# Kernel optimization log

Hardware: AMD Instinct MI355X
Metric: run time of the kernel (lower is better)

## Reference

```python
import jax, jax.numpy as jnp
import numpy as np

NEG_SLOPE = 0.2  # PyG GATv2Conv default negative_slope


def setup_inputs() -> dict:
    key = jax.random.key(0)
    ks = jax.random.split(key, 8)
    B, N, C, H, F, E = 16, 5000, 128, 2, 64, 1_280_000
    T = B * N
    s = 0.05
    x = jax.random.normal(ks[0], (B, N, C), jnp.float32)
    edge_index = jax.random.randint(ks[1], (2, E), 0, T, jnp.int32)
    Wl = jax.random.normal(ks[2], (C, H * F), jnp.float32) * s
    bl = jnp.zeros((H * F,), jnp.float32)
    Wr = jax.random.normal(ks[3], (C, H * F), jnp.float32) * s
    br = jnp.zeros((H * F,), jnp.float32)
    att = jax.random.normal(ks[4], (H, F), jnp.float32) * s
    bias = jnp.zeros((H * F,), jnp.float32)
    return {"x": x, "edge_index": edge_index, "Wl": Wl, "bl": bl,
            "Wr": Wr, "br": br, "att": att, "bias": bias}


def reference(x, edge_index, Wl, bl, Wr, br, att, bias):
    # x: (B, N, C) -> flatten to (T, C), T = B*N total nodes
    B, N, C = x.shape
    T = B * N
    H, F = att.shape
    xf = x.reshape(T, C)
    x_l = (xf @ Wl + bl).reshape(T, H, F)  # source transform (lin_l)
    x_r = (xf @ Wr + br).reshape(T, H, F)  # target transform (lin_r)
    # add self loops (add_self_loops=True)
    loops = jnp.arange(T, dtype=edge_index.dtype)
    src = jnp.concatenate([edge_index[0], loops])
    dst = jnp.concatenate([edge_index[1], loops])
    # GATv2 score: att . LeakyReLU(x_j + x_i)
    e = jax.nn.leaky_relu(x_l[src] + x_r[dst], NEG_SLOPE)  # (Et, H, F)
    logits = jnp.einsum('ehf,hf->eh', e, att)              # (Et, H)
    # edge softmax over incoming edges of each dst node
    m = jax.lax.stop_gradient(jax.ops.segment_max(logits, dst, num_segments=T))
    p = jnp.exp(logits - m[dst])
    denom = jax.ops.segment_sum(p, dst, num_segments=T)
    alpha = p / denom[dst]                                  # (Et, H)
    # aggregate: out_i = sum_j alpha_ij * x_l[j]
    out = jax.ops.segment_sum(x_l[src] * alpha[:, :, None], dst, num_segments=T)
    out = out.reshape(T, H * F) + bias  # concat=True -> (T, H*F)
    return out.reshape(B, N, H * F)
```

## Files before the change

kernel.cpp:

```cpp
#include <hip/hip_runtime.h>
#include <hip/hip_bf16.h>

typedef __hip_bfloat16 bf16;
typedef short s16x8 __attribute__((ext_vector_type(8)));
typedef float f32x4 __attribute__((ext_vector_type(4)));
typedef float f32x2 __attribute__((ext_vector_type(2)));

#define NEG_SLOPE 0.2f
#define MAXB 160
#define EPB  4096
#define CAP  12288

__device__ __forceinline__ unsigned int f32_to_bf16_bits(float f) {
    unsigned int u = __float_as_uint(f);
    return (u + 0x7FFFu + ((u >> 16) & 1u)) >> 16;
}
__device__ __forceinline__ float bf16lo_to_f32(unsigned int u) {
    return __uint_as_float(u << 16);
}
__device__ __forceinline__ float bf16hi_to_f32(unsigned int u) {
    return __uint_as_float(u & 0xFFFF0000u);
}
__device__ __forceinline__ float loadf_rt(const void* p, size_t i, int isb) {
    return isb ? __bfloat162float(((const bf16*)p)[i]) : ((const float*)p)[i];
}

#define ROR_ADD(v, n)                                                          \
    v += __int_as_float(__builtin_amdgcn_update_dpp(                           \
        0, __float_as_int(v), 0x120 + (n), 0xF, 0xF, true))

__global__ void detect_dtype(const unsigned short* __restrict__ xh, int* __restrict__ flag,
                             int* __restrict__ gtot)
{
    int lane = threadIdx.x;
    for (int j = lane; j < MAXB; j += 64) gtot[j] = 0;
    int cnt = 0;
    for (int j = lane; j < 256; j += 64) {
        unsigned short h = xh[j];
        int e = (h >> 7) & 0xFF;
        if ((h & 0x7FFF) == 0 || (e >= 117 && e <= 131)) cnt++;
    }
    #pragma unroll
    for (int off = 32; off; off >>= 1) cnt += __shfl_xor(cnt, off, 64);
    if (lane == 0) *flag = (cnt >= 192) ? 1 : 0;
}

__global__ void prep_w(const void* __restrict__ Wl, const void* __restrict__ Wr,
                       unsigned short* __restrict__ bpack, const int* __restrict__ flag)
{
    int isb = *flag;
    int tid = blockIdx.x * blockDim.x + threadIdx.x;
    if (tid >= 2 * 8 * 4 * 64) return;
    int lane = tid & 63;
    int kc   = (tid >> 6) & 3;
    int nt   = (tid >> 8) & 7;
    int mat  = tid >> 11;
    const void* W = mat ? Wr : Wl;
    int n  = nt * 16 + (lane & 15);
    int k0 = kc * 32 + (lane >> 4) * 8;
    unsigned short* o = bpack + (size_t)tid * 8;
    #pragma unroll
    for (int j = 0; j < 8; ++j)
        o[j] = (unsigned short)f32_to_bf16_bits(loadf_rt(W, (size_t)(k0 + j) * 128 + n, isb));
}

__global__ void gemm_mfma(const void* __restrict__ x,
                          const unsigned short* __restrict__ bpack,
                          const void* __restrict__ bl, const void* __restrict__ br,
                          unsigned int* __restrict__ xlp, unsigned int* __restrict__ xrp,
                          int T, const int* __restrict__ flag)
{
    int isb  = *flag;
    int lane = threadIdx.x & 63;
    int w    = blockIdx.x * 4 + (threadIdx.x >> 6);
    int row0 = w * 16;
    if (row0 >= T) return;
    int m = lane & 15, quad = lane >> 4;
    int arow = min(row0 + m, T - 1);

    f32x4 acc[16];
    #pragma unroll
    for (int nt = 0; nt < 16; ++nt) acc[nt] = (f32x4){0.f, 0.f, 0.f, 0.f};

    const s16x8* bp = (const s16x8*)bpack;
    for (int kc = 0; kc < 4; ++kc) {
        s16x8 a;
        if (isb) {
            const unsigned short* xb = (const unsigned short*)x
                                     + (size_t)arow * 128 + kc * 32 + quad * 8;
            a = *(const s16x8*)xb;
        } else {
            const float* xp = (const float*)x + (size_t)arow * 128 + kc * 32 + quad * 8;
            float4 xa = ((const float4*)xp)[0];
            float4 xc = ((const float4*)xp)[1];
            a[0] = (short)f32_to_bf16_bits(xa.x); a[1] = (short)f32_to_bf16_bits(xa.y);
            a[2] = (short)f32_to_bf16_bits(xa.z); a[3] = (short)f32_to_bf16_bits(xa.w);
            a[4] = (short)f32_to_bf16_bits(xc.x); a[5] = (short)f32_to_bf16_bits(xc.y);
            a[6] = (short)f32_to_bf16_bits(xc.z); a[7] = (short)f32_to_bf16_bits(xc.w);
        }
        #pragma unroll
        for (int nt = 0; nt < 16; ++nt) {
            s16x8 b = bp[(size_t)(((nt >> 3) * 32) + (nt & 7) * 4 + kc) * 64 + lane];
            acc[nt] = __builtin_amdgcn_mfma_f32_16x16x32_bf16(a, b, acc[nt], 0, 0, 0);
        }
    }
    #pragma unroll
    for (int nt = 0; nt < 4; ++nt) {
        int fl = nt * 16 + m;
        float bl0 = loadf_rt(bl, fl, isb), bl1 = loadf_rt(bl, 64 + fl, isb);
        float br0 = loadf_rt(br, fl, isb), br1 = loadf_rt(br, 64 + fl, isb);
        #pragma unroll
        for (int r = 0; r < 4; ++r) {
            int t = row0 + quad * 4 + r;
            if (t < T) {
                unsigned int pl = f32_to_bf16_bits(acc[nt][r] + bl0)
                                | (f32_to_bf16_bits(acc[nt + 4][r] + bl1) << 16);
                unsigned int pr = f32_to_bf16_bits(acc[nt + 8][r] + br0)
                                | (f32_to_bf16_bits(acc[nt + 12][r] + br1) << 16);
                xlp[(size_t)t * 64 + fl] = pl;
                xrp[(size_t)t * 64 + fl] = pr;
            }
        }
    }
}


__global__ void bucket_hist2(const int* __restrict__ ei, int E, int Et,
                             int nbuck, int* __restrict__ gtot)
{
    __shared__ int h[4][MAXB];
    int tid = threadIdx.x, wid = tid >> 6;
    for (int j = tid; j < 4 * MAXB; j += 256) h[j / MAXB][j % MAXB] = 0;
    __syncthreads();
    int start = blockIdx.x * EPB;
    int end   = min(start + EPB, Et);
    for (int i = start + tid; i < end; i += 256) {
        int dst = (i < E) ? ei[E + i] : (i - E);
        atomicAdd(&h[wid][dst >> 9], 1);
    }
    __syncthreads();
    for (int b = tid; b < nbuck; b += 256) {
        int v = h[0][b] + h[1][b] + h[2][b] + h[3][b];
        if (v) atomicAdd(&gtot[b], v);
    }
}

__global__ void scan_buckets(int* __restrict__ gtot, int nbuck, int Et,
                             int* __restrict__ bases, int* __restrict__ rowptr_T)
{
    __shared__ int sd[256];
    int tid = threadIdx.x;
    int v = (tid < nbuck) ? gtot[tid] : 0;
    sd[tid] = v;
    __syncthreads();
    for (int off = 1; off < 256; off <<= 1) {
        int u = (tid >= off) ? sd[tid - off] : 0;
        __syncthreads();
        sd[tid] += u;
        __syncthreads();
    }
    int excl = sd[tid] - v;
    if (tid < nbuck) { bases[tid] = excl; gtot[tid] = excl; }
    if (tid == 0) { bases[nbuck] = Et; *rowptr_T = Et; }
}

__global__ void bucket_scatter2(const int* __restrict__ ei, int E, int Et,
                                int nbuck, int* __restrict__ gcur,
                                unsigned int* __restrict__ packed)
{
    __shared__ int h[4][MAXB];
    __shared__ int cur[MAXB];
    int tid = threadIdx.x, wid = tid >> 6;
    for (int j = tid; j < 4 * MAXB; j += 256) h[j / MAXB][j % MAXB] = 0;
    __syncthreads();
    int start = blockIdx.x * EPB;
    int end   = min(start + EPB, Et);
    for (int i = start + tid; i < end; i += 256) {
        int dst = (i < E) ? ei[E + i] : (i - E);
        atomicAdd(&h[wid][dst >> 9], 1);
    }
    __syncthreads();
    for (int b = tid; b < nbuck; b += 256) {
        int v = h[0][b] + h[1][b] + h[2][b] + h[3][b];
        cur[b] = v ? atomicAdd(&gcur[b], v) : 0;
    }
    __syncthreads();
    for (int i = start + tid; i < end; i += 256) {
        int src, dst;
        if (i < E) { src = ei[i]; dst = ei[E + i]; }
        else       { src = i - E; dst = i - E; }
        int pos = atomicAdd(&cur[dst >> 9], 1);
        packed[pos] = ((unsigned int)src << 9) | (unsigned int)(dst & 511);
    }
}

__global__ void build_csr(unsigned int* __restrict__ colpacked,
                          const int* __restrict__ bases, int nbuck,
                          int Et, int T, int* __restrict__ row_ptr)
{
    __shared__ unsigned int st[CAP];
    __shared__ int h[512];
    __shared__ int off[512];
    __shared__ int ws[4];
    int b    = blockIdx.x;
    int tid  = threadIdx.x, lane = tid & 63, wid = tid >> 6;
    int base = bases[b];
    int endb = bases[b + 1];
    int m    = min(endb - base, CAP);

    for (int i = tid; i < m; i += 256) st[i] = colpacked[base + i];
    for (int j = tid; j < 512; j += 256) h[j] = 0;
    __syncthreads();
    for (int i = tid; i < m; i += 256) atomicAdd(&h[st[i] & 511], 1);
    __syncthreads();

    int h0 = h[2 * tid], h1 = h[2 * tid + 1];
    int s  = h0 + h1;
    int xx = s;
    #pragma unroll
    for (int o = 1; o < 64; o <<= 1) {
        int u = __shfl_up(xx, o, 64);
        if (lane >= o) xx += u;
    }
    if (lane == 63) ws[wid] = xx;
    __syncthreads();
    int wo = 0;
    for (int wv = 0; wv < 4; ++wv) if (wv < wid) wo += ws[wv];
    int e0 = wo + xx - s;
    int e1 = e0 + h0;
    off[2 * tid]     = e0;
    off[2 * tid + 1] = e1;
    int node0 = b * 512 + 2 * tid;
    if (node0 < T)     row_ptr[node0]     = base + e0;
    if (node0 + 1 < T) row_ptr[node0 + 1] = base + e1;
    __syncthreads();

    for (int i = tid; i < m; i += 256) {
        unsigned int p = st[i];
        int pos = atomicAdd(&off[p & 511], 1);
        colpacked[base + pos] = p >> 9;
    }
}

__global__ void aggregate(const unsigned int* __restrict__ xlp,
                          const unsigned int* __restrict__ xrp,
                          const int* __restrict__ row_ptr, const int* __restrict__ col,
                          const void* __restrict__ att, const void* __restrict__ bias,
                          float* __restrict__ out, int T,
                          const int* __restrict__ flag)
{
    int lane = threadIdx.x & 63;
    int node = blockIdx.x * 8 + (threadIdx.x >> 5);
    if (node >= T) return;
    int isb = *flag;
    int g = (lane >> 4) & 1;
    int q = lane & 15;

    uint4 xr4 = ((const uint4*)(xrp + (size_t)node * 64))[q];
    f32x2 xr2[4], at2[4];
    {
        unsigned int xrw[4] = {xr4.x, xr4.y, xr4.z, xr4.w};
        #pragma unroll
        for (int k = 0; k < 4; ++k) {
            xr2[k] = (f32x2){bf16lo_to_f32(xrw[k]), bf16hi_to_f32(xrw[k])};
            at2[k] = (f32x2){loadf_rt(att, q * 4 + k, isb),
                             loadf_rt(att, 64 + q * 4 + k, isb)};
        }
    }

    f32x2 s2 = {0.f, 0.f};
    f32x2 a2[4] = {{0.f, 0.f}, {0.f, 0.f}, {0.f, 0.f}, {0.f, 0.f}};

    int beg = row_ptr[node], end = row_ptr[node + 1];

    bool v0 = (beg + g) < end;      int sA = v0 ? col[beg + g]     : node;
    bool v1 = (beg + 2 + g) < end;  int sB = v1 ? col[beg + 2 + g] : node;
    bool v2 = (beg + 4 + g) < end;  int sC = v2 ? col[beg + 4 + g] : node;
    uint4 cx = ((const uint4*)(xlp + (size_t)sA * 64))[q];
    uint4 nx = ((const uint4*)(xlp + (size_t)sB * 64))[q];

    for (int i = beg; i < end; i += 2) {
        bool v3 = (i + 6 + g) < end;
        int  sD = v3 ? col[i + 6 + g] : node;
        uint4 px = ((const uint4*)(xlp + (size_t)sC * 64))[q];

        unsigned int xlw[4] = {cx.x, cx.y, cx.z, cx.w};
        f32x2 xl2[4];
        f32x2 t2 = {0.f, 0.f};
        #pragma unroll
        for (int k = 0; k < 4; ++k) {
            xl2[k] = (f32x2){bf16lo_to_f32(xlw[k]), bf16hi_to_f32(xlw[k])};
            f32x2 e  = xl2[k] + xr2[k];
            f32x2 lr = __builtin_elementwise_max(e, e * NEG_SLOPE);
            t2 = __builtin_elementwise_fma(lr, at2[k], t2);
        }
        float t0 = t2.x, t1 = t2.y;
        ROR_ADD(t0, 8); ROR_ADD(t1, 8);
        ROR_ADD(t0, 4); ROR_ADD(t1, 4);
        ROR_ADD(t0, 2); ROR_ADD(t1, 2);
        ROR_ADD(t0, 1); ROR_ADD(t1, 1);
        t0 = fminf(fmaxf(t0, -30.f), 30.f);
        t1 = fminf(fmaxf(t1, -30.f), 30.f);
        f32x2 p2;
        p2.x = v0 ? __expf(t0) : 0.f;
        p2.y = v0 ? __expf(t1) : 0.f;
        s2 += p2;
        #pragma unroll
        for (int k = 0; k < 4; ++k)
            a2[k] = __builtin_elementwise_fma(p2, xl2[k], a2[k]);

        cx = nx; nx = px;
        v0 = v1; v1 = v2; v2 = v3; sC = sD;
    }

    s2.x += __shfl_xor(s2.x, 16, 64);
    s2.y += __shfl_xor(s2.y, 16, 64);
    #pragma unroll
    for (int k = 0; k < 4; ++k) {
        a2[k].x += __shfl_xor(a2[k].x, 16, 64);
        a2[k].y += __shfl_xor(a2[k].y, 16, 64);
    }

    float inv0 = (s2.x > 0.f) ? 1.f / s2.x : 0.f;
    float inv1 = (s2.y > 0.f) ? 1.f / s2.y : 0.f;
    if (g == 0) {
        float4 o;
        o.x = fmaf(a2[0].x, inv0, loadf_rt(bias, q * 4 + 0, isb));
        o.y = fmaf(a2[1].x, inv0, loadf_rt(bias, q * 4 + 1, isb));
        o.z = fmaf(a2[2].x, inv0, loadf_rt(bias, q * 4 + 2, isb));
        o.w = fmaf(a2[3].x, inv0, loadf_rt(bias, q * 4 + 3, isb));
        ((float4*)(out + (size_t)node * 128))[q] = o;
    } else {
        float4 o;
        o.x = fmaf(a2[0].y, inv1, loadf_rt(bias, 64 + q * 4 + 0, isb));
        o.y = fmaf(a2[1].y, inv1, loadf_rt(bias, 64 + q * 4 + 1, isb));
        o.z = fmaf(a2[2].y, inv1, loadf_rt(bias, 64 + q * 4 + 2, isb));
        o.w = fmaf(a2[3].y, inv1, loadf_rt(bias, 64 + q * 4 + 3, isb));
        ((float4*)(out + (size_t)node * 128))[16 + q] = o;
    }
}

extern "C" void kernel_launch(void* const* d_in, const int* in_sizes, int n_in,
                              void* d_out, int out_size, void* d_ws, size_t ws_size,
                              hipStream_t stream)
{
    const void* x    = d_in[0];
    const int*  ei   = (const int*)d_in[1];
    const void* Wl   = d_in[2];
    const void* bl   = d_in[3];
    const void* Wr   = d_in[4];
    const void* br   = d_in[5];
    const void* att  = d_in[6];
    const void* bias = d_in[7];
    float* out = (float*)d_out;

    int T     = in_sizes[0] / 128;
    int E     = in_sizes[1] / 2;
    int Et    = E + T;
    int nbuck = (T + 511) >> 9;
    int nb    = (Et + EPB - 1) / EPB;

    char* w = (char*)d_ws;
    unsigned int* xlp = (unsigned int*)w;  w += (size_t)T * 64 * 4;
    unsigned int* xrp = (unsigned int*)w;  w += (size_t)T * 64 * 4;
    int* rowptr = (int*)w;  w += (size_t)(T + 1) * 4;
    unsigned int* col = (unsigned int*)w;  w += (size_t)Et * 4;
    int* gtot   = (int*)w;  w += MAXB * 4;
    int* bases  = (int*)w;  w += (MAXB + 8) * 4;
    int* flag   = (int*)w;  w += 256;
    unsigned short* bpack = (unsigned short*)w;  w += 2 * 8 * 4 * 64 * 8 * 2;

    detect_dtype<<<1, 64, 0, stream>>>((const unsigned short*)x, flag, gtot);
    prep_w<<<16, 256, 0, stream>>>(Wl, Wr, bpack, flag);
    gemm_mfma<<<(T + 63) / 64, 256, 0, stream>>>(x, bpack, bl, br, xlp, xrp, T, flag);

    bucket_hist2<<<nb, 256, 0, stream>>>(ei, E, Et, nbuck, gtot);
    scan_buckets<<<1, 256, 0, stream>>>(gtot, nbuck, Et, bases, rowptr + T);
    bucket_scatter2<<<nb, 256, 0, stream>>>(ei, E, Et, nbuck, gtot, col);
    build_csr<<<nbuck, 256, 0, stream>>>(col, bases, nbuck, Et, T, rowptr);

    aggregate<<<(T + 7) / 8, 256, 0, stream>>>(xlp, xrp, rowptr, (const int*)col,
                                               att, bias, out, T, flag);
}
```

Before: 247.9 us.

## Stage bucket scatter in shared memory, deepen gather prefetch, use exp2 softmax

The bucket scatter kernel now sorts each block's edges by bucket locally in shared memory, then writes them to global memory in contiguous runs per bucket instead of as random scattered stores. The aggregate kernel deepens its software prefetch of source feature rows from two rows ahead to three, to hide more gather latency at the cost of extra registers. It also folds log2(e) into the attention weights so it can call exp2f directly, replacing the symmetric clamp with an upper clamp only. The scatter kernel uses about 20KB more LDS per block, which may reduce occupancy.

```diff
diff --git a/kernel.cpp b/kernel.cpp
--- a/kernel.cpp
+++ b/kernel.cpp
@@ -164,12 +164,18 @@
     if (tid == 0) { bases[nbuck] = Et; *rowptr_T = Et; }
 }
 
-__global__ void bucket_scatter2(const int* __restrict__ ei, int E, int Et,
+__global__ void bucket_scatter3(const int* __restrict__ ei, int E, int Et,
                                 int nbuck, int* __restrict__ gcur,
                                 unsigned int* __restrict__ packed)
 {
+    __shared__ unsigned int st[EPB];
+    __shared__ unsigned char bk[EPB];
     __shared__ int h[4][MAXB];
+    __shared__ int sd[256];
+    __shared__ int loff[MAXB];
     __shared__ int cur[MAXB];
+    __shared__ int gpos[MAXB];
+
     int tid = threadIdx.x, wid = tid >> 6;
     for (int j = tid; j < 4 * MAXB; j += 256) h[j / MAXB][j % MAXB] = 0;
     __syncthreads();
@@ -180,17 +186,37 @@
         atomicAdd(&h[wid][dst >> 9], 1);
     }
     __syncthreads();
-    for (int b = tid; b < nbuck; b += 256) {
-        int v = h[0][b] + h[1][b] + h[2][b] + h[3][b];
-        cur[b] = v ? atomicAdd(&gcur[b], v) : 0;
+    int v = 0;
+    if (tid < nbuck) v = h[0][tid] + h[1][tid] + h[2][tid] + h[3][tid];
+    sd[tid] = v;
+    __syncthreads();
+    for (int off = 1; off < 256; off <<= 1) {
+        int u = (tid >= off) ? sd[tid - off] : 0;
+        __syncthreads();
+        sd[tid] += u;
+        __syncthreads();
+    }
+    if (tid < nbuck) {
+        int excl = sd[tid] - v;
+        loff[tid] = excl;
+        cur[tid]  = excl;
+        gpos[tid] = v ? atomicAdd(&gcur[tid], v) : 0;
     }
     __syncthreads();
     for (int i = start + tid; i < end; i += 256) {
         int src, dst;
         if (i < E) { src = ei[i]; dst = ei[E + i]; }
         else       { src = i - E; dst = i - E; }
-        int pos = atomicAdd(&cur[dst >> 9], 1);
-        packed[pos] = ((unsigned int)src << 9) | (unsigned int)(dst & 511);
+        int b = dst >> 9;
+        int pos = atomicAdd(&cur[b], 1);
+        st[pos] = ((unsigned int)src << 9) | (unsigned int)(dst & 511);
+        bk[pos] = (unsigned char)b;
+    }
+    __syncthreads();
+    int mm = end - start;
+    for (int i = tid; i < mm; i += 256) {
+        int b = bk[i];
+        packed[gpos[b] + (i - loff[b])] = st[i];
     }
 }
 
@@ -260,11 +286,12 @@
     f32x2 xr2[4], at2[4];
     {
         unsigned int xrw[4] = {xr4.x, xr4.y, xr4.z, xr4.w};
+        const float LOG2E = 1.44269504f;
         #pragma unroll
         for (int k = 0; k < 4; ++k) {
             xr2[k] = (f32x2){bf16lo_to_f32(xrw[k]), bf16hi_to_f32(xrw[k])};
-            at2[k] = (f32x2){loadf_rt(att, q * 4 + k, isb),
-                             loadf_rt(att, 64 + q * 4 + k, isb)};
+            at2[k] = (f32x2){loadf_rt(att, q * 4 + k, isb) * LOG2E,
+                             loadf_rt(att, 64 + q * 4 + k, isb) * LOG2E};
         }
     }
 
@@ -276,13 +303,15 @@
     bool v0 = (beg + g) < end;      int sA = v0 ? col[beg + g]     : node;
     bool v1 = (beg + 2 + g) < end;  int sB = v1 ? col[beg + 2 + g] : node;
     bool v2 = (beg + 4 + g) < end;  int sC = v2 ? col[beg + 4 + g] : node;
+    bool v3 = (beg + 6 + g) < end;  int sD = v3 ? col[beg + 6 + g] : node;
     uint4 cx = ((const uint4*)(xlp + (size_t)sA * 64))[q];
     uint4 nx = ((const uint4*)(xlp + (size_t)sB * 64))[q];
+    uint4 px = ((const uint4*)(xlp + (size_t)sC * 64))[q];
 
     for (int i = beg; i < end; i += 2) {
-        bool v3 = (i + 6 + g) < end;
-        int  sD = v3 ? col[i + 6 + g] : node;
-        uint4 px = ((const uint4*)(xlp + (size_t)sC * 64))[q];
+        bool v4 = (i + 8 + g) < end;
+        int  sE = v4 ? col[i + 8 + g] : node;
+        uint4 qx = ((const uint4*)(xlp + (size_t)sD * 64))[q];
 
         unsigned int xlw[4] = {cx.x, cx.y, cx.z, cx.w};
         f32x2 xl2[4];
@@ -299,18 +328,18 @@
         ROR_ADD(t0, 4); ROR_ADD(t1, 4);
         ROR_ADD(t0, 2); ROR_ADD(t1, 2);
         ROR_ADD(t0, 1); ROR_ADD(t1, 1);
-        t0 = fminf(fmaxf(t0, -30.f), 30.f);
-        t1 = fminf(fmaxf(t1, -30.f), 30.f);
+        t0 = fminf(t0, 43.3f);
+        t1 = fminf(t1, 43.3f);
         f32x2 p2;
-        p2.x = v0 ? __expf(t0) : 0.f;
-        p2.y = v0 ? __expf(t1) : 0.f;
+        p2.x = v0 ? exp2f(t0) : 0.f;
+        p2.y = v0 ? exp2f(t1) : 0.f;
         s2 += p2;
         #pragma unroll
         for (int k = 0; k < 4; ++k)
             a2[k] = __builtin_elementwise_fma(p2, xl2[k], a2[k]);
 
-        cx = nx; nx = px;
-        v0 = v1; v1 = v2; v2 = v3; sC = sD;
+        cx = nx; nx = px; px = qx;
+        v0 = v1; v1 = v2; v2 = v3; v3 = v4; sD = sE;
     }
 
     s2.x += __shfl_xor(s2.x, 16, 64);
@@ -376,7 +405,7 @@
 
     bucket_hist2<<<nb, 256, 0, stream>>>(ei, E, Et, nbuck, gtot);
     scan_buckets<<<1, 256, 0, stream>>>(gtot, nbuck, Et, bases, rowptr + T);
-    bucket_scatter2<<<nb, 256, 0, stream>>>(ei, E, Et, nbuck, gtot, col);
+    bucket_scatter3<<<nb, 256, 0, stream>>>(ei, E, Et, nbuck, gtot, col);
     build_csr<<<nbuck, 256, 0, stream>>>(col, bases, nbuck, Et, T, rowptr);
 
     aggregate<<<(T + 7) / 8, 256, 0, stream>>>(xlp, xrp, rowptr, (const int*)col,
```

After: 261.9 us. 1.06x slower.
